# Performance work log

Hardware: AMD Instinct MI355X
Metric: run time of the kernel (lower is better)

The kernel has to match this reference:

```python
import jax, jax.numpy as jnp
import numpy as np

NU = 100000  # num user nodes
NI = 100000  # num item nodes
E = 1600000  # edges per edge type
L = 100000   # labeled edges
H = 128      # hidden_channels
EPS = 1e-12  # F.normalize eps


def sage_conv(x_src, x_dst, edge_index, w_l, b_l, w_r, num_dst):
    """PyG SAGEConv, mean aggregation, normalize=True.
    w_l, w_r: [H, H] stored as [in, out]; lin_r has no bias."""
    src, dst = edge_index[0], edge_index[1]
    msg_sum = jax.ops.segment_sum(x_src[src], dst, num_segments=num_dst)  # [num_dst, H]
    cnt = jax.ops.segment_sum(jnp.ones((src.shape[0],), x_src.dtype), dst, num_segments=num_dst)
    mean = msg_sum / jnp.maximum(cnt, 1.0)[:, None]
    out = mean @ w_l + b_l + x_dst @ w_r
    norm = jnp.sqrt(jnp.sum(out * out, axis=-1, keepdims=True))
    return out / jnp.maximum(norm, EPS)


def setup_inputs() -> dict:
    key = jax.random.key(0)
    ks = jax.random.split(key, 20)
    s = 1.0 / np.sqrt(H)
    d = {
        'emb_user': jax.random.normal(ks[0], (NU, H), jnp.float32),
        'emb_item': jax.random.normal(ks[1], (NI, H), jnp.float32),
        'edge_rates': jax.random.randint(ks[2], (2, E), 0, 100000, jnp.int32),
        'edge_rev': jax.random.randint(ks[3], (2, E), 0, 100000, jnp.int32),
        'edge_label_index': jax.random.randint(ks[4], (2, L), 0, 100000, jnp.int32),
    }
    names = ['w1l_rates', 'w1r_rates', 'w1l_rev', 'w1r_rev',
             'w2l_rates', 'w2r_rates', 'w2l_rev', 'w2r_rev']
    for i, n in enumerate(names):
        d[n] = jax.random.uniform(ks[5 + i], (H, H), jnp.float32, -s, s)
    for i, n in enumerate(['b1_rates', 'b1_rev', 'b2_rates', 'b2_rev']):
        d[n] = jax.random.uniform(ks[13 + i], (H,), jnp.float32, -s, s)
    return d


def reference(emb_user, emb_item, edge_rates, edge_rev, edge_label_index,
              w1l_rates, w1r_rates, w1l_rev, w1r_rev,
              w2l_rates, w2r_rates, w2l_rev, w2r_rev,
              b1_rates, b1_rev, b2_rates, b2_rev):
    xu, xi = emb_user, emb_item
    # layer 1: each node type receives exactly one edge type (HeteroConv mean is identity)
    xi1 = sage_conv(xu, xi, edge_rates, w1l_rates, b1_rates, w1r_rates, NI)
    xu1 = sage_conv(xi, xu, edge_rev, w1l_rev, b1_rev, w1r_rev, NU)
    xu1 = jax.nn.relu(xu1)  # dropout is identity in eval mode
    xi1 = jax.nn.relu(xi1)
    # layer 2
    xi2 = sage_conv(xu1, xi1, edge_rates, w2l_rates, b2_rates, w2r_rates, NI)
    xu2 = sage_conv(xi1, xu1, edge_rev, w2l_rev, b2_rev, w2r_rev, NU)
    xu2 = jax.nn.relu(xu2)
    xi2 = jax.nn.relu(xi2)
    # classifier: dot(user[src], item[dst])
    x_src = xu2[edge_label_index[0]]
    x_dst = xi2[edge_label_index[1]]
    return jnp.sum(x_src * x_dst, axis=-1)
```

## Files before the change

### kernel.cpp

```cpp
#include <hip/hip_runtime.h>
#include <hip/hip_bf16.h>

#define NUM_U 100000
#define NUM_I 100000
#define NE    1600000
#define NL    100000
#define CAP   48
#define NBIN  391
#define BINCAP 4608
#define ROUND  4096

typedef __attribute__((ext_vector_type(4))) float floatx4;
typedef __attribute__((ext_vector_type(8))) short shortx8;
typedef unsigned long long u64;

__device__ __forceinline__ float bf_lo(unsigned v) { return __uint_as_float(v << 16); }
__device__ __forceinline__ float bf_hi(unsigned v) { return __uint_as_float(v & 0xffff0000u); }

__device__ __forceinline__ unsigned pack_bf16x2(float lo, float hi) {
    __hip_bfloat16 l = __float2bfloat16(lo);
    __hip_bfloat16 h = __float2bfloat16(hi);
    unsigned short ul = *(unsigned short*)&l;
    unsigned short uh = *(unsigned short*)&h;
    return (unsigned)ul | ((unsigned)uh << 16);
}

__device__ __forceinline__ int clampi(int x, int hi) {
    return min(max(x, 0), hi - 1);
}

__global__ void zero_kernel(int* __restrict__ p, int n) {
    int i = blockIdx.x * blockDim.x + threadIdx.x;
    if (i < n) p[i] = 0;
}

__global__ void zero_f32_kernel(float* __restrict__ p, int n) {
    int i = blockIdx.x * blockDim.x + threadIdx.x;
    if (i < n) p[i] = 0.0f;
}

__global__ void conv_bf16_kernel(const float* __restrict__ in, unsigned* __restrict__ out,
                                 int n_pairs) {
    int i = blockIdx.x * blockDim.x + threadIdx.x;
    if (i >= n_pairs) return;
    float2 v = ((const float2*)in)[i];
    out[i] = pack_bf16x2(v.x, v.y);
}

__global__ __launch_bounds__(256) void partition_kernel(
    const int* __restrict__ edges, u64* __restrict__ bin_data,
    int* __restrict__ bin_cursor, int nE) {
    __shared__ int hist[NBIN];
    __shared__ int prefix[NBIN];
    __shared__ int gbase[NBIN];
    __shared__ __align__(16) u64 sorted[ROUND];

    const int tid  = threadIdx.x;
    const int lane = tid & 63;
    const int wv   = tid >> 6;
    const int base = blockIdx.x * ROUND;

    for (int k = tid; k < NBIN; k += 256) hist[k] = 0;
    __syncthreads();

    int mybin[16], myrank[16], mysrc[16], mydst[16];
#pragma unroll
    for (int r = 0; r < 16; r++) {
        int i = base + r * 256 + tid;
        mybin[r] = -1;
        if (i < nE) {
            mysrc[r] = clampi(edges[i], NUM_U);
            mydst[r] = clampi(edges[i + nE], NUM_I);
            mybin[r] = mydst[r] >> 8;
            myrank[r] = atomicAdd(&hist[mybin[r]], 1);
        }
    }
    __syncthreads();

    if (wv == 0) {
        int carry = 0;
        for (int c = 0; c < NBIN; c += 64) {
            int idx = c + lane;
            int h = (idx < NBIN) ? hist[idx] : 0;
            int v = h;
            for (int o = 1; o < 64; o <<= 1) {
                int t = __shfl_up(v, o);
                if (lane >= o) v += t;
            }
            if (idx < NBIN) prefix[idx] = v - h + carry;
            carry += __shfl(v, 63);
        }
    }
    __syncthreads();

#pragma unroll
    for (int r = 0; r < 16; r++) {
        if (mybin[r] >= 0) {
            int j = prefix[mybin[r]] + myrank[r];
            sorted[j] = ((u64)(unsigned)mydst[r] << 32) | (unsigned)mysrc[r];
        }
    }
    __syncthreads();

    for (int b = tid; b < NBIN; b += 256) {
        int cnt = hist[b];
        gbase[b] = (cnt > 0) ? atomicAdd(&bin_cursor[b], cnt) : 0;
    }
    __syncthreads();

    int total = min(ROUND, nE - base);
    for (int j = tid; j < total; j += 256) {
        u64 e = sorted[j];
        int b = (int)(e >> 40);
        int pos = gbase[b] + (j - prefix[b]);
        if (pos < BINCAP)
            bin_data[(size_t)b * BINCAP + pos] = e;
    }
}

__global__ __launch_bounds__(256) void binscatter_kernel(
    const u64* __restrict__ bin_data, const int* __restrict__ bin_cursor,
    int* __restrict__ deg, int* __restrict__ bucket, int n_dst) {
    __shared__ int lbucket[256 * CAP];
    __shared__ int ldeg[256];
    const int tid = threadIdx.x;
    const int b = blockIdx.x;
    const int dstbase = b << 8;

    ldeg[tid] = 0;
    __syncthreads();

    int count = min(bin_cursor[b], BINCAP);
    for (int j = tid; j < count; j += 256) {
        u64 e = bin_data[(size_t)b * BINCAP + j];
        int src = (int)(unsigned)e;
        int dl = ((int)(e >> 32)) & 255;
        int pos = atomicAdd(&ldeg[dl], 1);
        if (pos < CAP) lbucket[dl * CAP + pos] = src;
    }
    __syncthreads();

    if (dstbase + tid < n_dst) deg[dstbase + tid] = ldeg[tid];
    int limit = min(256, n_dst - dstbase) * CAP;
    for (int k = tid; k < limit; k += 256)
        bucket[(size_t)dstbase * CAP + k] = lbucket[k];
}

__global__ __launch_bounds__(256) void agg_kernel(
    const int* __restrict__ deg, const int* __restrict__ bucket,
    const unsigned* __restrict__ xb, unsigned* __restrict__ mean_out, int n_dst) {
    int wave = (blockIdx.x * blockDim.x + threadIdx.x) >> 6;
    int lane = threadIdx.x & 63;
    if (wave >= n_dst) return;
    int d = deg[wave];
    int cnt = min(d, CAP);
    int srcs = (lane < cnt) ? bucket[wave * CAP + lane] : 0;
    float a0 = 0.f, a1 = 0.f;
    int e = 0;
    for (; e + 4 <= cnt; e += 4) {
        int s0 = __shfl(srcs, e);
        int s1 = __shfl(srcs, e + 1);
        int s2 = __shfl(srcs, e + 2);
        int s3 = __shfl(srcs, e + 3);
        unsigned v0 = xb[(size_t)s0 * 64 + lane];
        unsigned v1 = xb[(size_t)s1 * 64 + lane];
        unsigned v2 = xb[(size_t)s2 * 64 + lane];
        unsigned v3 = xb[(size_t)s3 * 64 + lane];
        a0 += bf_lo(v0) + bf_lo(v1) + bf_lo(v2) + bf_lo(v3);
        a1 += bf_hi(v0) + bf_hi(v1) + bf_hi(v2) + bf_hi(v3);
    }
    for (; e < cnt; e++) {
        int s0 = __shfl(srcs, e);
        unsigned v0 = xb[(size_t)s0 * 64 + lane];
        a0 += bf_lo(v0); a1 += bf_hi(v0);
    }
    float scale = 1.0f / (float)max(d, 1);
    mean_out[(size_t)wave * 64 + lane] = pack_bf16x2(a0 * scale, a1 * scale);
}

__global__ void transpose_w4_kernel(
    const float* __restrict__ w1l_rates, const float* __restrict__ w1r_rates,
    const float* __restrict__ w1l_rev,   const float* __restrict__ w1r_rev,
    const float* __restrict__ w2l_rates, const float* __restrict__ w2r_rates,
    const float* __restrict__ w2l_rev,   const float* __restrict__ w2r_rev,
    short* __restrict__ Bt) {
    int idx = blockIdx.x * blockDim.x + threadIdx.x;
    int which = idx >> 15;
    int r = idx & 32767;
    int n = r >> 8;
    int k = r & 255;
    const float *wl, *wr;
    switch (which) {
        case 0:  wl = w1l_rates; wr = w1r_rates; break;
        case 1:  wl = w1l_rev;   wr = w1r_rev;   break;
        case 2:  wl = w2l_rates; wr = w2r_rates; break;
        default: wl = w2l_rev;   wr = w2r_rev;   break;
    }
    float v = (k < 128) ? wl[k * 128 + n] : wr[(k - 128) * 128 + n];
    __hip_bfloat16 b = __float2bfloat16(v);
    Bt[idx] = *(const short*)&b;
}

__global__ __launch_bounds__(256) void sage_fused_kernel(
    const unsigned* __restrict__ meanb,
    const unsigned* __restrict__ xdstb,
    const short* __restrict__ Bt,
    const float* __restrict__ bias,
    unsigned* __restrict__ outb,
    int n_rows) {
    __shared__ __align__(16) short A_lds[128 * 72];
    __shared__ float rowsum[128][2];

    const int tid  = threadIdx.x;
    const int lane = tid & 63;
    const int wv   = tid >> 6;
    const int wm   = wv >> 1;
    const int wn   = wv & 1;
    const int rb   = blockIdx.x * 128;
    const int l15  = lane & 15;
    const int lq   = lane >> 4;

    floatx4 acc[4][4];
#pragma unroll
    for (int nt = 0; nt < 4; nt++) {
        float b = bias[wn * 64 + nt * 16 + l15];
#pragma unroll
        for (int mt = 0; mt < 4; mt++) acc[mt][nt] = (floatx4){b, b, b, b};
    }

    for (int kt = 0; kt < 4; kt++) {
        __syncthreads();
        const unsigned* srcbuf = (kt < 2) ? meanb : xdstb;
        const int kbase_u = (kt & 1) * 32;
#pragma unroll
        for (int j = 0; j < 4; j++) {
            int c = tid + j * 256;
            int row = c >> 3;
            int kc = (c & 7) * 8;
            int grow = rb + row;
            uint4 v = make_uint4(0u, 0u, 0u, 0u);
            if (grow < n_rows)
                v = *(const uint4*)(srcbuf + (size_t)grow * 64 + kbase_u + (kc >> 1));
            *(uint4*)&A_lds[row * 72 + kc] = v;
        }
        __syncthreads();

#pragma unroll
        for (int kk = 0; kk < 64; kk += 32) {
            shortx8 af[4], bfr[4];
#pragma unroll
            for (int mt = 0; mt < 4; mt++) {
                int row_l = wm * 64 + mt * 16 + l15;
                af[mt] = *(const shortx8*)&A_lds[row_l * 72 + kk + lq * 8];
            }
#pragma unroll
            for (int nt = 0; nt < 4; nt++) {
                int col = wn * 64 + nt * 16 + l15;
                int kg = kt * 64 + kk + lq * 8;
                bfr[nt] = *(const shortx8*)(Bt + col * 256 + kg);
            }
#pragma unroll
            for (int mt = 0; mt < 4; mt++)
#pragma unroll
                for (int nt = 0; nt < 4; nt++)
                    acc[mt][nt] = __builtin_amdgcn_mfma_f32_16x16x32_bf16(
                        af[mt], bfr[nt], acc[mt][nt], 0, 0, 0);
        }
    }

#pragma unroll
    for (int mt = 0; mt < 4; mt++) {
#pragma unroll
        for (int r = 0; r < 4; r++) {
            float p = 0.f;
#pragma unroll
            for (int nt = 0; nt < 4; nt++) { float x = acc[mt][nt][r]; p += x * x; }
            for (int o = 1; o < 16; o <<= 1) p += __shfl_xor(p, o);
            if (l15 == 0) rowsum[wm * 64 + mt * 16 + lq * 4 + r][wn] = p;
        }
    }
    __syncthreads();

#pragma unroll
    for (int mt = 0; mt < 4; mt++) {
#pragma unroll
        for (int r = 0; r < 4; r++) {
            int row_l = wm * 64 + mt * 16 + lq * 4 + r;
            int grow = rb + row_l;
            float s = rowsum[row_l][0] + rowsum[row_l][1];
            float inv = 1.f / fmaxf(sqrtf(s), 1e-12f);
#pragma unroll
            for (int nt = 0; nt < 4; nt++) {
                float v = fmaxf(acc[mt][nt][r] * inv, 0.f);
                float vnb = __shfl_xor(v, 1);
                if (grow < n_rows && (l15 & 1) == 0) {
                    int colpair = (wn * 64 + nt * 16 + l15) >> 1;
                    outb[(size_t)grow * 64 + colpair] = pack_bf16x2(v, vnb);
                }
            }
        }
    }
}

__global__ __launch_bounds__(256) void classifier_kernel(
    const unsigned* __restrict__ xu, const unsigned* __restrict__ xi,
    const int* __restrict__ eli, float* __restrict__ out, int nL) {
    int wave = (blockIdx.x * blockDim.x + threadIdx.x) >> 6;
    int lane = threadIdx.x & 63;
    if (wave >= nL) return;
    int su = clampi(eli[wave], NUM_U);
    int di = clampi(eli[wave + nL], NUM_I);
    unsigned a = xu[(size_t)su * 64 + lane];
    unsigned b = xi[(size_t)di * 64 + lane];
    float p = bf_lo(a) * bf_lo(b) + bf_hi(a) * bf_hi(b);
    for (int o = 32; o; o >>= 1) p += __shfl_xor(p, o);
    if (lane == 0) out[wave] = p;
}

extern "C" void kernel_launch(void* const* d_in, const int* in_sizes, int n_in,
                              void* d_out, int out_size, void* d_ws, size_t ws_size,
                              hipStream_t stream) {
    const float* emb_user = (const float*)d_in[0];
    const float* emb_item = (const float*)d_in[1];
    const int* edge_rates = (const int*)d_in[2];
    const int* edge_rev   = (const int*)d_in[3];
    const int* eli        = (const int*)d_in[4];
    const float* b1_rates = (const float*)d_in[13];
    const float* b1_rev   = (const float*)d_in[14];
    const float* b2_rates = (const float*)d_in[15];
    const float* b2_rev   = (const float*)d_in[16];

    char* p = (char*)d_ws;
    auto alloc = [&](size_t bytes) -> void* {
        void* q = (void*)p;
        p += (bytes + 511) & ~(size_t)511;
        return q;
    };
    int* deg_rates    = (int*)alloc((size_t)NUM_I * 4);
    int* bucket_rates = (int*)alloc((size_t)NUM_I * CAP * 4);
    int* deg_rev      = (int*)alloc((size_t)NUM_U * 4);
    int* bucket_rev   = (int*)alloc((size_t)NUM_U * CAP * 4);
    unsigned* meanI = (unsigned*)alloc((size_t)NUM_I * 64 * 4);
    unsigned* meanU = (unsigned*)alloc((size_t)NUM_U * 64 * 4);
    unsigned* xi    = (unsigned*)alloc((size_t)NUM_I * 64 * 4);
    unsigned* xu    = (unsigned*)alloc((size_t)NUM_U * 64 * 4);
    short* Bt = (short*)alloc((size_t)4 * 32768 * 2);
    int* bin_cursor = (int*)alloc((size_t)NBIN * 4);
    u64* bin_data = (u64*)meanI;

    const int partBlocks = (NE + ROUND - 1) / ROUND;
    const int aggBlocks  = (NUM_I * 64 + 255) / 256;
    const int gemmBlocks = (NUM_I + 127) / 128;
    const int convBlocks = (NUM_I * 64 + 255) / 256;

    if (out_size > NL) {
        int tail = out_size - NL;
        zero_f32_kernel<<<(tail + 255) / 256, 256, 0, stream>>>((float*)d_out + NL, tail);
    }

    transpose_w4_kernel<<<512, 256, 0, stream>>>(
        (const float*)d_in[5], (const float*)d_in[6],
        (const float*)d_in[7], (const float*)d_in[8],
        (const float*)d_in[9], (const float*)d_in[10],
        (const float*)d_in[11], (const float*)d_in[12], Bt);

    conv_bf16_kernel<<<convBlocks, 256, 0, stream>>>(emb_user, xu, NUM_U * 64);
    conv_bf16_kernel<<<convBlocks, 256, 0, stream>>>(emb_item, xi, NUM_I * 64);

    zero_kernel<<<2, 256, 0, stream>>>(bin_cursor, NBIN);
    partition_kernel<<<partBlocks, 256, 0, stream>>>(edge_rates, bin_data, bin_cursor, NE);
    binscatter_kernel<<<NBIN, 256, 0, stream>>>(bin_data, bin_cursor,
                                                deg_rates, bucket_rates, NUM_I);
    zero_kernel<<<2, 256, 0, stream>>>(bin_cursor, NBIN);
    partition_kernel<<<partBlocks, 256, 0, stream>>>(edge_rev, bin_data, bin_cursor, NE);
    binscatter_kernel<<<NBIN, 256, 0, stream>>>(bin_data, bin_cursor,
                                                deg_rev, bucket_rev, NUM_U);

    agg_kernel<<<aggBlocks, 256, 0, stream>>>(deg_rates, bucket_rates, xu, meanI, NUM_I);
    agg_kernel<<<aggBlocks, 256, 0, stream>>>(deg_rev, bucket_rev, xi, meanU, NUM_U);
    sage_fused_kernel<<<gemmBlocks, 256, 0, stream>>>(meanI, xi, Bt + 0 * 32768, b1_rates,
                                                      xi, NUM_I);
    sage_fused_kernel<<<gemmBlocks, 256, 0, stream>>>(meanU, xu, Bt + 1 * 32768, b1_rev,
                                                      xu, NUM_U);

    agg_kernel<<<aggBlocks, 256, 0, stream>>>(deg_rates, bucket_rates, xu, meanI, NUM_I);
    agg_kernel<<<aggBlocks, 256, 0, stream>>>(deg_rev, bucket_rev, xi, meanU, NUM_U);
    sage_fused_kernel<<<gemmBlocks, 256, 0, stream>>>(meanI, xi, Bt + 2 * 32768, b2_rates,
                                                      xi, NUM_I);
    sage_fused_kernel<<<gemmBlocks, 256, 0, stream>>>(meanU, xu, Bt + 3 * 32768, b2_rev,
                                                      xu, NUM_U);

    classifier_kernel<<<(NL * 64 + 255) / 256, 256, 0, stream>>>(xu, xi, eli,
                                                                 (float*)d_out, NL);
}
```

Measured before the change: 666.0 us.

## Merge per-edge-type kernel pairs into single launches across the pipeline

The paired launches for the two edge types (bf16 conversion, partition, binscatter, aggregation and fused GEMM) are each merged into one launch. Each block picks its edge type from its block index, and the cursor zeroing moves into the weight-transpose kernel. This cuts the launch count from about 17 to 9 and lets both edge types' work share the GPU at the same time, at the cost of a little branching per block. The two partitions now write to separate scratch buffers (meanI and meanU), and the aggregation and classifier outputs use nontemporal stores.

```diff
diff --git a/kernel.cpp b/kernel.cpp
--- a/kernel.cpp
+++ b/kernel.cpp
@@ -9,6 +9,7 @@
 #define NBIN  391
 #define BINCAP 4608
 #define ROUND  4096
+#define PB    391
 
 typedef __attribute__((ext_vector_type(4))) float floatx4;
 typedef __attribute__((ext_vector_type(8))) short shortx8;
@@ -29,36 +30,66 @@
     return min(max(x, 0), hi - 1);
 }
 
-__global__ void zero_kernel(int* __restrict__ p, int n) {
-    int i = blockIdx.x * blockDim.x + threadIdx.x;
-    if (i < n) p[i] = 0;
-}
-
 __global__ void zero_f32_kernel(float* __restrict__ p, int n) {
     int i = blockIdx.x * blockDim.x + threadIdx.x;
     if (i < n) p[i] = 0.0f;
 }
 
-__global__ void conv_bf16_kernel(const float* __restrict__ in, unsigned* __restrict__ out,
-                                 int n_pairs) {
+__global__ void conv2_kernel(const float* __restrict__ emb_u, const float* __restrict__ emb_i,
+                             unsigned* __restrict__ xu, unsigned* __restrict__ xi) {
     int i = blockIdx.x * blockDim.x + threadIdx.x;
-    if (i >= n_pairs) return;
-    float2 v = ((const float2*)in)[i];
-    out[i] = pack_bf16x2(v.x, v.y);
-}
-
-__global__ __launch_bounds__(256) void partition_kernel(
-    const int* __restrict__ edges, u64* __restrict__ bin_data,
-    int* __restrict__ bin_cursor, int nE) {
+    const int nu = NUM_U * 64;
+    if (i < nu) {
+        float2 v = ((const float2*)emb_u)[i];
+        xu[i] = pack_bf16x2(v.x, v.y);
+    } else if (i < nu + NUM_I * 64) {
+        int j = i - nu;
+        float2 v = ((const float2*)emb_i)[j];
+        xi[j] = pack_bf16x2(v.x, v.y);
+    }
+}
+
+__global__ void transpose_w4_kernel(
+    const float* __restrict__ w1l_rates, const float* __restrict__ w1r_rates,
+    const float* __restrict__ w1l_rev,   const float* __restrict__ w1r_rev,
+    const float* __restrict__ w2l_rates, const float* __restrict__ w2r_rates,
+    const float* __restrict__ w2l_rev,   const float* __restrict__ w2r_rev,
+    short* __restrict__ Bt, int* __restrict__ bin_cursor) {
+    int idx = blockIdx.x * blockDim.x + threadIdx.x;
+    if (idx < 2 * NBIN) bin_cursor[idx] = 0;
+    int which = idx >> 15;
+    int r = idx & 32767;
+    int n = r >> 8;
+    int k = r & 255;
+    const float *wl, *wr;
+    switch (which) {
+        case 0:  wl = w1l_rates; wr = w1r_rates; break;
+        case 1:  wl = w1l_rev;   wr = w1r_rev;   break;
+        case 2:  wl = w2l_rates; wr = w2r_rates; break;
+        default: wl = w2l_rev;   wr = w2r_rev;   break;
+    }
+    float v = (k < 128) ? wl[k * 128 + n] : wr[(k - 128) * 128 + n];
+    __hip_bfloat16 b = __float2bfloat16(v);
+    Bt[idx] = *(const short*)&b;
+}
+
+__global__ __launch_bounds__(256) void partition2_kernel(
+    const int* __restrict__ edges0, const int* __restrict__ edges1,
+    u64* __restrict__ bd0, u64* __restrict__ bd1, int* __restrict__ cur) {
     __shared__ int hist[NBIN];
     __shared__ int prefix[NBIN];
     __shared__ int gbase[NBIN];
     __shared__ __align__(16) u64 sorted[ROUND];
 
+    const int type = (blockIdx.x >= PB) ? 1 : 0;
+    const int* edges = type ? edges1 : edges0;
+    u64* bin_data = type ? bd1 : bd0;
+    int* bin_cursor = cur + type * NBIN;
+    const int blk  = blockIdx.x - type * PB;
     const int tid  = threadIdx.x;
     const int lane = tid & 63;
     const int wv   = tid >> 6;
-    const int base = blockIdx.x * ROUND;
+    const int base = blk * ROUND;
 
     for (int k = tid; k < NBIN; k += 256) hist[k] = 0;
     __syncthreads();
@@ -68,9 +99,9 @@
     for (int r = 0; r < 16; r++) {
         int i = base + r * 256 + tid;
         mybin[r] = -1;
-        if (i < nE) {
+        if (i < NE) {
             mysrc[r] = clampi(edges[i], NUM_U);
-            mydst[r] = clampi(edges[i + nE], NUM_I);
+            mydst[r] = clampi(edges[i + NE], NUM_I);
             mybin[r] = mydst[r] >> 8;
             myrank[r] = atomicAdd(&hist[mybin[r]], 1);
         }
@@ -108,7 +139,7 @@
     }
     __syncthreads();
 
-    int total = min(ROUND, nE - base);
+    int total = min(ROUND, NE - base);
     for (int j = tid; j < total; j += 256) {
         u64 e = sorted[j];
         int b = (int)(e >> 40);
@@ -118,19 +149,25 @@
     }
 }
 
-__global__ __launch_bounds__(256) void binscatter_kernel(
-    const u64* __restrict__ bin_data, const int* __restrict__ bin_cursor,
-    int* __restrict__ deg, int* __restrict__ bucket, int n_dst) {
+__global__ __launch_bounds__(256) void binscatter2_kernel(
+    const u64* __restrict__ bd0, const u64* __restrict__ bd1, const int* __restrict__ cur,
+    int* __restrict__ deg0, int* __restrict__ bucket0,
+    int* __restrict__ deg1, int* __restrict__ bucket1) {
     __shared__ int lbucket[256 * CAP];
     __shared__ int ldeg[256];
+    const int type = (blockIdx.x >= NBIN) ? 1 : 0;
+    const int b = blockIdx.x - type * NBIN;
+    const u64* bin_data = type ? bd1 : bd0;
+    int* deg = type ? deg1 : deg0;
+    int* bucket = type ? bucket1 : bucket0;
     const int tid = threadIdx.x;
-    const int b = blockIdx.x;
     const int dstbase = b << 8;
+    const int n_dst = NUM_I;
 
     ldeg[tid] = 0;
     __syncthreads();
 
-    int count = min(bin_cursor[b], BINCAP);
+    int count = min(cur[type * NBIN + b], BINCAP);
     for (int j = tid; j < count; j += 256) {
         u64 e = bin_data[(size_t)b * BINCAP + j];
         int src = (int)(unsigned)e;
@@ -146,15 +183,21 @@
         bucket[(size_t)dstbase * CAP + k] = lbucket[k];
 }
 
-__global__ __launch_bounds__(256) void agg_kernel(
-    const int* __restrict__ deg, const int* __restrict__ bucket,
-    const unsigned* __restrict__ xb, unsigned* __restrict__ mean_out, int n_dst) {
-    int wave = (blockIdx.x * blockDim.x + threadIdx.x) >> 6;
+__global__ __launch_bounds__(256) void agg2_kernel(
+    const int* __restrict__ degA, const int* __restrict__ bucketA,
+    const unsigned* __restrict__ xA, unsigned* __restrict__ outA,
+    const int* __restrict__ degB, const int* __restrict__ bucketB,
+    const unsigned* __restrict__ xB, unsigned* __restrict__ outB) {
+    int w = (blockIdx.x * blockDim.x + threadIdx.x) >> 6;
     int lane = threadIdx.x & 63;
-    if (wave >= n_dst) return;
-    int d = deg[wave];
+    const int* deg; const int* bucket; const unsigned* xb; unsigned* mo; int node;
+    if (w < NUM_I) { deg = degA; bucket = bucketA; xb = xA; mo = outA; node = w; }
+    else if (w < NUM_I + NUM_U) { deg = degB; bucket = bucketB; xb = xB; mo = outB; node = w - NUM_I; }
+    else return;
+
+    int d = deg[node];
     int cnt = min(d, CAP);
-    int srcs = (lane < cnt) ? bucket[wave * CAP + lane] : 0;
+    int srcs = (lane < cnt) ? bucket[node * CAP + lane] : 0;
     float a0 = 0.f, a1 = 0.f;
     int e = 0;
     for (; e + 4 <= cnt; e += 4) {
@@ -175,48 +218,33 @@
         a0 += bf_lo(v0); a1 += bf_hi(v0);
     }
     float scale = 1.0f / (float)max(d, 1);
-    mean_out[(size_t)wave * 64 + lane] = pack_bf16x2(a0 * scale, a1 * scale);
-}
-
-__global__ void transpose_w4_kernel(
-    const float* __restrict__ w1l_rates, const float* __restrict__ w1r_rates,
-    const float* __restrict__ w1l_rev,   const float* __restrict__ w1r_rev,
-    const float* __restrict__ w2l_rates, const float* __restrict__ w2r_rates,
-    const float* __restrict__ w2l_rev,   const float* __restrict__ w2r_rev,
-    short* __restrict__ Bt) {
-    int idx = blockIdx.x * blockDim.x + threadIdx.x;
-    int which = idx >> 15;
-    int r = idx & 32767;
-    int n = r >> 8;
-    int k = r & 255;
-    const float *wl, *wr;
-    switch (which) {
-        case 0:  wl = w1l_rates; wr = w1r_rates; break;
-        case 1:  wl = w1l_rev;   wr = w1r_rev;   break;
-        case 2:  wl = w2l_rates; wr = w2r_rates; break;
-        default: wl = w2l_rev;   wr = w2r_rev;   break;
-    }
-    float v = (k < 128) ? wl[k * 128 + n] : wr[(k - 128) * 128 + n];
-    __hip_bfloat16 b = __float2bfloat16(v);
-    Bt[idx] = *(const short*)&b;
-}
-
-__global__ __launch_bounds__(256) void sage_fused_kernel(
-    const unsigned* __restrict__ meanb,
-    const unsigned* __restrict__ xdstb,
-    const short* __restrict__ Bt,
-    const float* __restrict__ bias,
-    unsigned* __restrict__ outb,
-    int n_rows) {
+    __builtin_nontemporal_store(pack_bf16x2(a0 * scale, a1 * scale),
+                                &mo[(size_t)node * 64 + lane]);
+}
+
+__global__ __launch_bounds__(256) void gemm2_kernel(
+    const unsigned* __restrict__ meanA, unsigned* __restrict__ xA,
+    const short* __restrict__ BtA, const float* __restrict__ biasA,
+    const unsigned* __restrict__ meanB, unsigned* __restrict__ xB,
+    const short* __restrict__ BtB, const float* __restrict__ biasB,
+    int nblocksA) {
     __shared__ __align__(16) short A_lds[128 * 72];
     __shared__ float rowsum[128][2];
+
+    const int half = (blockIdx.x >= nblocksA) ? 1 : 0;
+    const unsigned* meanb = half ? meanB : meanA;
+    const unsigned* xdstb = half ? xB : xA;
+    unsigned* outb = half ? xB : xA;
+    const short* Bt = half ? BtB : BtA;
+    const float* bias = half ? biasB : biasA;
+    const int rb = (blockIdx.x - half * nblocksA) * 128;
+    const int n_rows = NUM_I;
 
     const int tid  = threadIdx.x;
     const int lane = tid & 63;
     const int wv   = tid >> 6;
     const int wm   = wv >> 1;
     const int wn   = wv & 1;
-    const int rb   = blockIdx.x * 128;
     const int l15  = lane & 15;
     const int lq   = lane >> 4;
 
@@ -314,7 +342,7 @@
     unsigned b = xi[(size_t)di * 64 + lane];
     float p = bf_lo(a) * bf_lo(b) + bf_hi(a) * bf_hi(b);
     for (int o = 32; o; o >>= 1) p += __shfl_xor(p, o);
-    if (lane == 0) out[wave] = p;
+    if (lane == 0) __builtin_nontemporal_store(p, &out[wave]);
 }
 
 extern "C" void kernel_launch(void* const* d_in, const int* in_sizes, int n_in,
@@ -345,13 +373,13 @@
     unsigned* xi    = (unsigned*)alloc((size_t)NUM_I * 64 * 4);
     unsigned* xu    = (unsigned*)alloc((size_t)NUM_U * 64 * 4);
     short* Bt = (short*)alloc((size_t)4 * 32768 * 2);
-    int* bin_cursor = (int*)alloc((size_t)NBIN * 4);
-    u64* bin_data = (u64*)meanI;
-
-    const int partBlocks = (NE + ROUND - 1) / ROUND;
-    const int aggBlocks  = (NUM_I * 64 + 255) / 256;
+    int* bin_cursor = (int*)alloc((size_t)2 * NBIN * 4);
+    u64* bd0 = (u64*)meanI;
+    u64* bd1 = (u64*)meanU;
+
     const int gemmBlocks = (NUM_I + 127) / 128;
-    const int convBlocks = (NUM_I * 64 + 255) / 256;
+    const int agg2Blocks = ((NUM_I + NUM_U) * 64 + 255) / 256;
+    const int conv2Blocks = ((NUM_U + NUM_I) * 64 + 255) / 256;
 
     if (out_size > NL) {
         int tail = out_size - NL;
@@ -362,33 +390,24 @@
         (const float*)d_in[5], (const float*)d_in[6],
         (const float*)d_in[7], (const float*)d_in[8],
         (const float*)d_in[9], (const float*)d_in[10],
-        (const float*)d_in[11], (const float*)d_in[12], Bt);
-
-    conv_bf16_kernel<<<convBlocks, 256, 0, stream>>>(emb_user, xu, NUM_U * 64);
-    conv_bf16_kernel<<<convBlocks, 256, 0, stream>>>(emb_item, xi, NUM_I * 64);
-
-    zero_kernel<<<2, 256, 0, stream>>>(bin_cursor, NBIN);
-    partition_kernel<<<partBlocks, 256, 0, stream>>>(edge_rates, bin_data, bin_cursor, NE);
-    binscatter_kernel<<<NBIN, 256, 0, stream>>>(bin_data, bin_cursor,
-                                                deg_rates, bucket_rates, NUM_I);
-    zero_kernel<<<2, 256, 0, stream>>>(bin_cursor, NBIN);
-    partition_kernel<<<partBlocks, 256, 0, stream>>>(edge_rev, bin_data, bin_cursor, NE);
-    binscatter_kernel<<<NBIN, 256, 0, stream>>>(bin_data, bin_cursor,
-                                                deg_rev, bucket_rev, NUM_U);
-
-    agg_kernel<<<aggBlocks, 256, 0, stream>>>(deg_rates, bucket_rates, xu, meanI, NUM_I);
-    agg_kernel<<<aggBlocks, 256, 0, stream>>>(deg_rev, bucket_rev, xi, meanU, NUM_U);
-    sage_fused_kernel<<<gemmBlocks, 256, 0, stream>>>(meanI, xi, Bt + 0 * 32768, b1_rates,
-                                                      xi, NUM_I);
-    sage_fused_kernel<<<gemmBlocks, 256, 0, stream>>>(meanU, xu, Bt + 1 * 32768, b1_rev,
-                                                      xu, NUM_U);
-
-    agg_kernel<<<aggBlocks, 256, 0, stream>>>(deg_rates, bucket_rates, xu, meanI, NUM_I);
-    agg_kernel<<<aggBlocks, 256, 0, stream>>>(deg_rev, bucket_rev, xi, meanU, NUM_U);
-    sage_fused_kernel<<<gemmBlocks, 256, 0, stream>>>(meanI, xi, Bt + 2 * 32768, b2_rates,
-                                                      xi, NUM_I);
-    sage_fused_kernel<<<gemmBlocks, 256, 0, stream>>>(meanU, xu, Bt + 3 * 32768, b2_rev,
-                                                      xu, NUM_U);
+        (const float*)d_in[11], (const float*)d_in[12], Bt, bin_cursor);
+    conv2_kernel<<<conv2Blocks, 256, 0, stream>>>(emb_user, emb_item, xu, xi);
+    partition2_kernel<<<2 * PB, 256, 0, stream>>>(edge_rates, edge_rev, bd0, bd1, bin_cursor);
+    binscatter2_kernel<<<2 * NBIN, 256, 0, stream>>>(bd0, bd1, bin_cursor,
+                                                     deg_rates, bucket_rates,
+                                                     deg_rev, bucket_rev);
+
+    agg2_kernel<<<agg2Blocks, 256, 0, stream>>>(deg_rates, bucket_rates, xu, meanI,
+                                                deg_rev, bucket_rev, xi, meanU);
+    gemm2_kernel<<<2 * gemmBlocks, 256, 0, stream>>>(meanI, xi, Bt + 0 * 32768, b1_rates,
+                                                     meanU, xu, Bt + 1 * 32768, b1_rev,
+                                                     gemmBlocks);
+
+    agg2_kernel<<<agg2Blocks, 256, 0, stream>>>(deg_rates, bucket_rates, xu, meanI,
+                                                deg_rev, bucket_rev, xi, meanU);
+    gemm2_kernel<<<2 * gemmBlocks, 256, 0, stream>>>(meanI, xi, Bt + 2 * 32768, b2_rates,
+                                                     meanU, xu, Bt + 3 * 32768, b2_rev,
+                                                     gemmBlocks);
 
     classifier_kernel<<<(NL * 64 + 255) / 256, 256, 0, stream>>>(xu, xi, eli,
                                                                  (float*)d_out, NL);
```

After: 637.4 us. 4.3% less time.
